# Performance work log

Hardware: AMD Instinct MI355X
Metric: run time of the kernel (lower is better)

Reference implementation:

```python
import jax, jax.numpy as jnp
import numpy as np

# ---- config (mirrors RPN __init__ + TEST proposal config) ----
B, DIN, CH, H, W = 4, 1024, 512, 50, 76
STRIDE = 16
PRE_NMS, POST_NMS = 6000, 300
NMS_THRESH, MIN_SIZE = 0.7, 16.0


def _generate_anchor_bases(base_size=16, ratios=np.array([0.5, 1.0, 2.0]), scales=np.array([8.0, 16.0, 32.0])):
    """Standard py-faster-rcnn generate_anchors."""
    def whctrs(a):
        w = a[2] - a[0] + 1.0
        h = a[3] - a[1] + 1.0
        return w, h, a[0] + 0.5 * (w - 1.0), a[1] + 0.5 * (h - 1.0)

    def mk(ws, hs, xc, yc):
        ws = ws[:, None]; hs = hs[:, None]
        return np.hstack([xc - 0.5 * (ws - 1), yc - 0.5 * (hs - 1),
                          xc + 0.5 * (ws - 1), yc + 0.5 * (hs - 1)])

    base = np.array([0.0, 0.0, base_size - 1.0, base_size - 1.0])
    w, h, xc, yc = whctrs(base)
    size = w * h
    ws = np.round(np.sqrt(size / ratios)); hs = np.round(ws * ratios)
    ratio_anchors = mk(ws, hs, xc, yc)
    out = []
    for i in range(ratio_anchors.shape[0]):
        w, h, xc, yc = whctrs(ratio_anchors[i])
        out.append(mk(w * scales, h * scales, xc, yc))
    return np.vstack(out).astype(np.float32)

ANCHOR_BASES = _generate_anchor_bases()  # [A,4]
A = ANCHOR_BASES.shape[0]                # 9


def setup_inputs() -> dict:
    keys = jax.random.split(jax.random.key(0), 4)
    base_feat = jax.random.normal(keys[0], (B, DIN, H, W), jnp.float32)
    im_info = jnp.tile(jnp.array([H * STRIDE, W * STRIDE, 1.0], jnp.float32), (B, 1))  # (im_h, im_w, scale)
    gt_boxes = jnp.zeros((B, 20, 5), jnp.float32)  # unused by forward
    num_boxes = jnp.zeros((B,), jnp.int32)         # unused by forward
    conv_w = jax.random.normal(keys[1], (CH, DIN, 3, 3), jnp.float32) * (1.0 / np.sqrt(DIN * 9))
    conv_b = jnp.zeros((CH,), jnp.float32)
    cls_w = jax.random.normal(keys[2], (2 * A, CH, 1, 1), jnp.float32) * 0.01
    cls_b = jnp.zeros((2 * A,), jnp.float32)
    bbox_w = jax.random.normal(keys[3], (4 * A, CH, 1, 1), jnp.float32) * 0.01
    bbox_b = jnp.zeros((4 * A,), jnp.float32)
    return dict(base_feat=base_feat, im_info=im_info, gt_boxes=gt_boxes, num_boxes=num_boxes,
                conv_w=conv_w, conv_b=conv_b, cls_w=cls_w, cls_b=cls_b, bbox_w=bbox_w, bbox_b=bbox_b)


def _greedy_nms(boxes, scores, n_keep, thresh):
    # boxes [N,4] (already sorted candidates), scores [N]; returns keep indices [n_keep]
    areas = (boxes[:, 2] - boxes[:, 0] + 1.0) * (boxes[:, 3] - boxes[:, 1] + 1.0)

    def body(i, st):
        sm, keep = st
        j = jnp.argmax(sm)
        keep = keep.at[i].set(j.astype(jnp.int32))
        b = boxes[j]
        xx1 = jnp.maximum(b[0], boxes[:, 0]); yy1 = jnp.maximum(b[1], boxes[:, 1])
        xx2 = jnp.minimum(b[2], boxes[:, 2]); yy2 = jnp.minimum(b[3], boxes[:, 3])
        inter = jnp.maximum(0.0, xx2 - xx1 + 1.0) * jnp.maximum(0.0, yy2 - yy1 + 1.0)
        iou = inter / (areas[j] + areas - inter)
        sm = jnp.where(iou > thresh, -jnp.inf, sm)  # suppresses j itself too (IoU=1)
        return sm, keep

    _, keep = jax.lax.fori_loop(0, n_keep, body, (scores, jnp.zeros((n_keep,), jnp.int32)))
    return keep


def reference(base_feat, im_info, gt_boxes, num_boxes, conv_w, conv_b, cls_w, cls_b, bbox_w, bbox_b):
    # 3x3 conv + relu
    x = jax.lax.conv_general_dilated(base_feat, conv_w, (1, 1), 'SAME',
                                     dimension_numbers=('NCHW', 'OIHW', 'NCHW'))
    x = jax.nn.relu(x + conv_b[None, :, None, None])
    # 1x1 heads
    cls = jnp.einsum('bchw,oc->bohw', x, cls_w[:, :, 0, 0]) + cls_b[None, :, None, None]   # [B,2A,H,W]
    bbox = jnp.einsum('bchw,oc->bohw', x, bbox_w[:, :, 0, 0]) + bbox_b[None, :, None, None]  # [B,4A,H,W]
    Bn, _, Hn, Wn = cls.shape
    # reshape(x,2)+softmax(dim=1)+reshape back == softmax over the (bg,fg) pair per anchor
    prob = jax.nn.softmax(cls.reshape(Bn, 2, A, Hn, Wn), axis=1)
    fg = prob[:, 1].transpose(0, 2, 3, 1).reshape(Bn, -1)            # [B, H*W*A], (h,w,a) order
    deltas = bbox.transpose(0, 2, 3, 1).reshape(Bn, -1, 4)           # [B, H*W*A, 4]

    # anchors in (h,w,a) order to match score/delta layout
    sy, sx = jnp.meshgrid(jnp.arange(Hn, dtype=jnp.float32) * STRIDE,
                          jnp.arange(Wn, dtype=jnp.float32) * STRIDE, indexing='ij')
    shifts = jnp.stack([sx, sy, sx, sy], -1)                         # [H,W,4]
    anchors = (shifts[:, :, None, :] + jnp.asarray(ANCHOR_BASES)[None, None]).reshape(-1, 4)
    aw = anchors[:, 2] - anchors[:, 0] + 1.0
    ah = anchors[:, 3] - anchors[:, 1] + 1.0
    axc = anchors[:, 0] + 0.5 * aw
    ayc = anchors[:, 1] + 0.5 * ah

    def per_image(scores, dl, info):
        # bbox_transform_inv
        cx = axc + dl[:, 0] * aw
        cy = ayc + dl[:, 1] * ah
        pw = jnp.exp(dl[:, 2]) * aw
        ph = jnp.exp(dl[:, 3]) * ah
        x1 = cx - 0.5 * pw; y1 = cy - 0.5 * ph
        x2 = cx + 0.5 * pw; y2 = cy + 0.5 * ph
        # clip to image
        x1 = jnp.clip(x1, 0.0, info[1] - 1.0); x2 = jnp.clip(x2, 0.0, info[1] - 1.0)
        y1 = jnp.clip(y1, 0.0, info[0] - 1.0); y2 = jnp.clip(y2, 0.0, info[0] - 1.0)
        # min_size filter (mask instead of removal to keep shapes static)
        ws = x2 - x1 + 1.0; hs = y2 - y1 + 1.0
        ms = MIN_SIZE * info[2]
        sc = jnp.where((ws >= ms) & (hs >= ms), scores, -jnp.inf)
        # pre-NMS top-k
        sc_top, idx = jax.lax.top_k(sc, PRE_NMS)
        boxes_k = jnp.stack([x1, y1, x2, y2], -1)[idx]               # [PRE_NMS,4]
        keep = _greedy_nms(boxes_k, sc_top, POST_NMS, NMS_THRESH)
        return sc_top[keep], boxes_k[keep]

    rpn_scores, rpn_bbox = jax.vmap(per_image)(fg, deltas, im_info)
    return rpn_scores[..., None], rpn_bbox  # [B,POST_NMS,1], [B,POST_NMS,4]
```

## Files before the change

kernel.cpp:

```cpp
#include <hip/hip_runtime.h>
#include <cstdint>
#include <math.h>

#define NBATCH 4
#define HH 50
#define WW 76
#define HWPIX 3800
#define HPAD 3840
#define NPROP 34200
#define NSORT 65536
#define PRE 6000
#define POST 300
#define NWORD 94
#define NROWP 6016

typedef double double4v __attribute__((ext_vector_type(4)));

__device__ __constant__ double d_AB[9][4] = {
  {-84.0,-40.0,99.0,55.0},
  {-176.0,-88.0,191.0,103.0},
  {-360.0,-184.0,375.0,199.0},
  {-56.0,-56.0,71.0,71.0},
  {-120.0,-120.0,135.0,135.0},
  {-248.0,-248.0,263.0,263.0},
  {-36.0,-80.0,51.0,95.0},
  {-80.0,-168.0,95.0,183.0},
  {-168.0,-344.0,183.0,359.0}
};

__global__ void transpose_w(const float* __restrict__ src, float* __restrict__ dst){
  __shared__ float t[32][33];
  const int kb = blockIdx.x*32, ob = blockIdx.y*32;
  const int lx = threadIdx.x, ly = threadIdx.y;
  #pragma unroll
  for (int m = 0; m < 32; m += 8){
    t[ly+m][lx] = src[(size_t)(ob+ly+m)*9216 + kb + lx];
  }
  __syncthreads();
  #pragma unroll
  for (int m = 0; m < 32; m += 8){
    dst[(size_t)(kb+ly+m)*512 + ob + lx] = t[lx][ly+m];
  }
}

__global__ void prep_head_w(const float* __restrict__ cls_w, const float* __restrict__ bbox_w,
                            float* __restrict__ wh){
  int g = blockIdx.x*256 + threadIdx.x;
  if (g >= 512*64) return;
  int c = g >> 6, o = g & 63;
  float v = 0.0f;
  if (o < 18) v = cls_w[o*512 + c];
  else if (o < 54) v = bbox_w[(o-18)*512 + c];
  wh[g] = v;
}

__global__ __launch_bounds__(256, 3) void conv3x3_mfma(
    const float* __restrict__ in, const float* __restrict__ wt,
    const float* __restrict__ bias, float* __restrict__ xout)
{
  __shared__ __align__(16) double wA[2][2304];
  __shared__ __align__(16) double iA[2][504];
  const int tid  = threadIdx.x;
  const int wave = tid >> 6, lane = tid & 63;
  const int kq = lane >> 4;
  const int ln = lane & 15;
  const int sp = blockIdx.x;
  const int rt = sp / 5, ct = sp - rt*5;
  const int y0 = rt*5, x0 = ct*16;
  const int ocb = blockIdx.y;
  const int b = blockIdx.z;
  const float* inb = in + (size_t)b*1024*HWPIX;

  int orow[4], ocol[4];
  {
    double pa  = (double)(1 << ln);
    double msk = (kq == 0) ? 1.0 : 0.0;
    double4v z = {0.0, 0.0, 0.0, 0.0};
    double4v d1 = __builtin_amdgcn_mfma_f64_16x16x4f64(pa,  msk, z, 0, 0, 0);
    double4v d2 = __builtin_amdgcn_mfma_f64_16x16x4f64(msk, pa,  z, 0, 0, 0);
    #pragma unroll
    for (int e = 0; e < 4; ++e){
      orow[e] = (int)(((__double_as_longlong(d1[e]) >> 52) & 0x7FF) - 1023);
      ocol[e] = (int)(((__double_as_longlong(d2[e]) >> 52) & 0x7FF) - 1023);
    }
  }

  double4v acc[5];
  #pragma unroll
  for (int r = 0; r < 5; ++r){ acc[r][0]=0.0; acc[r][1]=0.0; acc[r][2]=0.0; acc[r][3]=0.0; }

  float wr[9], ir[2];

  auto load_chunk = [&](int icb){
    #pragma unroll
    for (int s = 0; s < 9; ++s){
      int m = tid + s*256;
      int row = m >> 6, oc = m & 63;
      wr[s] = wt[(size_t)(icb*9 + row)*512 + ocb*64 + oc];
    }
    #pragma unroll
    for (int s = 0; s < 2; ++s){
      int m = tid + s*256;
      if (m < 504){
        int ic = m/126; int rem = m - ic*126;
        int ry = rem/18; int rx = rem - ry*18;
        int y = y0 - 1 + ry; int x = x0 - 1 + rx;
        ir[s] = ((unsigned)y < (unsigned)HH && (unsigned)x < (unsigned)WW)
                  ? inb[(size_t)(icb+ic)*HWPIX + y*WW + x] : 0.0f;
      }
    }
  };
  auto store_chunk = [&](int buf){
    #pragma unroll
    for (int s = 0; s < 9; ++s) wA[buf][tid + s*256] = (double)wr[s];
    #pragma unroll
    for (int s = 0; s < 2; ++s){
      int m = tid + s*256;
      if (m < 504) iA[buf][m] = (double)ir[s];
    }
  };

  load_chunk(0);
  store_chunk(0);
  load_chunk(4);
  __syncthreads();

  #pragma unroll 1
  for (int c = 0; c < 256; ++c){
    const int cur = c & 1;
    if (c + 1 < 256){
      store_chunk(1 - cur);
      if (c + 2 < 256) load_chunk((c + 2)*4);
    }
    #pragma unroll
    for (int tap = 0; tap < 9; ++tap){
      const int ky = tap/3, kx = tap - ky*3;
      double a = wA[cur][(kq*9 + tap)*64 + wave*16 + ln];
      #pragma unroll
      for (int rr = 0; rr < 5; ++rr){
        double bb = iA[cur][kq*126 + (rr+ky)*18 + ln + kx];
        acc[rr] = __builtin_amdgcn_mfma_f64_16x16x4f64(a, bb, acc[rr], 0, 0, 0);
      }
    }
    __syncthreads();
  }

  #pragma unroll
  for (int rr = 0; rr < 5; ++rr){
    const int y = y0 + rr;
    #pragma unroll
    for (int e = 0; e < 4; ++e){
      const int oc = ocb*64 + wave*16 + orow[e];
      const int xx = x0 + ocol[e];
      if (xx < WW){
        double val = fmax(acc[rr][e] + (double)bias[oc], 0.0);
        xout[((size_t)b*512 + oc)*HWPIX + y*WW + xx] = (float)val;
      }
    }
  }
}

__global__ __launch_bounds__(256) void head_mm(const float* __restrict__ x,
    const float* __restrict__ wh, double* __restrict__ hout)
{
  __shared__ float xs[32*128];
  __shared__ float wls[32*64];
  const int tid = threadIdx.x;
  const int b = blockIdx.y;
  const int p0 = blockIdx.x*128;
  const int oct = tid >> 5;
  const int pq = tid & 31;
  double acc[8][4];
  #pragma unroll
  for (int k=0;k<8;++k){
    #pragma unroll
    for (int j=0;j<4;++j) acc[k][j]=0.0;
  }
  const float* xb = x + (size_t)b*512*HWPIX;
  #pragma unroll 1
  for (int cb = 0; cb < 512; cb += 32){
    for (int m = tid; m < 4096; m += 256){
      int cc = m >> 7; int px = m & 127;
      int p = p0 + px;
      xs[m] = (p < HWPIX) ? xb[(size_t)(cb+cc)*HWPIX + p] : 0.0f;
    }
    for (int m = tid; m < 2048; m += 256)
      wls[m] = wh[(size_t)(cb + (m >> 6))*64 + (m & 63)];
    __syncthreads();
    #pragma unroll 1
    for (int cc = 0; cc < 32; ++cc){
      const float4 xv = *(const float4*)&xs[cc*128 + pq*4];
      double xd0 = (double)xv.x, xd1 = (double)xv.y, xd2 = (double)xv.z, xd3 = (double)xv.w;
      const float* wp = &wls[cc*64 + oct*8];
      #pragma unroll
      for (int k = 0; k < 8; ++k){
        double w = (double)wp[k];
        acc[k][0] = fma(w, xd0, acc[k][0]);
        acc[k][1] = fma(w, xd1, acc[k][1]);
        acc[k][2] = fma(w, xd2, acc[k][2]);
        acc[k][3] = fma(w, xd3, acc[k][3]);
      }
    }
    __syncthreads();
  }
  #pragma unroll
  for (int k = 0; k < 8; ++k){
    #pragma unroll
    for (int j = 0; j < 4; ++j)
      hout[((size_t)b*64 + oct*8 + k)*HPAD + p0 + pq*4 + j] = acc[k][j];
  }
}

__global__ void decode_boxes(const double* __restrict__ hout, const float* __restrict__ im_info,
    const float* __restrict__ cls_b, const float* __restrict__ bbox_b,
    double* __restrict__ sc, double* __restrict__ bxs, ulonglong2* __restrict__ keys)
{
  int g = blockIdx.x*256 + threadIdx.x;
  int b = g >> 16;
  int n = g & 65535;
  if (b >= NBATCH) return;
  ulonglong2 kv;
  if (n < NPROP){
    int p = n / 9; int a = n - p*9;
    int yr = p / WW; int xc = p - yr*WW;
    const double* hb = hout + (size_t)b*64*HPAD;
    double l0 = hb[(size_t)a*HPAD + p] + (double)cls_b[a];
    double l1 = hb[(size_t)(9+a)*HPAD + p] + (double)cls_b[9+a];
    double score = 1.0/(1.0 + exp(l0 - l1));
    double d0 = hb[(size_t)(18+4*a+0)*HPAD+p] + (double)bbox_b[4*a+0];
    double d1 = hb[(size_t)(18+4*a+1)*HPAD+p] + (double)bbox_b[4*a+1];
    double d2 = hb[(size_t)(18+4*a+2)*HPAD+p] + (double)bbox_b[4*a+2];
    double d3 = hb[(size_t)(18+4*a+3)*HPAD+p] + (double)bbox_b[4*a+3];
    double sx = 16.0*xc, sy = 16.0*yr;
    double ax1 = d_AB[a][0]+sx, ay1 = d_AB[a][1]+sy;
    double ax2 = d_AB[a][2]+sx, ay2 = d_AB[a][3]+sy;
    double aw = ax2-ax1+1.0, ah = ay2-ay1+1.0;
    double axc = ax1+0.5*aw, ayc = ay1+0.5*ah;
    double cx = axc + d0*aw, cy = ayc + d1*ah;
    double pw = exp(d2)*aw, ph = exp(d3)*ah;
    double i0 = (double)im_info[b*3+0];
    double i1 = (double)im_info[b*3+1];
    double i2 = (double)im_info[b*3+2];
    double x1 = cx - 0.5*pw, y1 = cy - 0.5*ph;
    double x2 = cx + 0.5*pw, y2 = cy + 0.5*ph;
    x1 = fmin(fmax(x1, 0.0), i1-1.0);
    x2 = fmin(fmax(x2, 0.0), i1-1.0);
    y1 = fmin(fmax(y1, 0.0), i0-1.0);
    y2 = fmin(fmax(y2, 0.0), i0-1.0);
    double wsz = x2-x1+1.0, hsz = y2-y1+1.0;
    double ms = 16.0*i2;
    double s = (wsz >= ms && hsz >= ms) ? score : -INFINITY;
    sc[(size_t)b*NPROP + n] = s;
    double* bp = bxs + ((size_t)b*NPROP + n)*4;
    bp[0]=x1; bp[1]=y1; bp[2]=x2; bp[3]=y2;
    unsigned long long u = (unsigned long long)__double_as_longlong(s);
    unsigned long long mm = (u >> 63) ? ~u : (u | 0x8000000000000000ULL);
    kv.x = ~mm; kv.y = (unsigned long long)n;
  } else {
    kv.x = ~0ULL; kv.y = (unsigned long long)n;
  }
  keys[(size_t)b*NSORT + n] = kv;
}

__device__ __forceinline__ bool kgt(const ulonglong2& a, const ulonglong2& b){
  return (a.x > b.x) || (a.x == b.x && a.y > b.y);
}
__global__ __launch_bounds__(1024) void sort_local(ulonglong2* __restrict__ keys){
  const int c = blockIdx.x & 31;
  const int b = blockIdx.x >> 5;
  ulonglong2* base = keys + (size_t)b*NSORT + c*2048;
  __shared__ ulonglong2 L[2048];
  const int tid = threadIdx.x;
  L[tid] = base[tid]; L[tid+1024] = base[tid+1024];
  __syncthreads();
  for (int k = 2; k <= 2048; k <<= 1){
    for (int j = k>>1; j > 0; j >>= 1){
      int i = ((tid & ~(j-1)) << 1) | (tid & (j-1));
      int l = i | j;
      bool asc = (((c*2048 + i) & k) == 0);
      ulonglong2 A = L[i], Bv = L[l];
      if (kgt(A,Bv) == asc){ L[i] = Bv; L[l] = A; }
      __syncthreads();
    }
  }
  base[tid] = L[tid]; base[tid+1024] = L[tid+1024];
}
__global__ void sort_gstep(ulonglong2* __restrict__ keys, int k, int j){
  int gid = blockIdx.x*256 + threadIdx.x;
  int b = gid >> 15;
  int q = gid & 32767;
  ulonglong2* base = keys + (size_t)b*NSORT;
  int i = ((q & ~(j-1)) << 1) | (q & (j-1));
  int l = i | j;
  bool asc = ((i & k) == 0);
  ulonglong2 A = base[i], Bv = base[l];
  if (kgt(A,Bv) == asc){ base[i] = Bv; base[l] = A; }
}
__global__ __launch_bounds__(1024) void sort_lmerge(ulonglong2* __restrict__ keys, int k){
  const int c = blockIdx.x & 31;
  const int b = blockIdx.x >> 5;
  ulonglong2* base = keys + (size_t)b*NSORT + c*2048;
  __shared__ ulonglong2 L[2048];
  const int tid = threadIdx.x;
  L[tid] = base[tid]; L[tid+1024] = base[tid+1024];
  __syncthreads();
  for (int j = 1024; j > 0; j >>= 1){
    int i = ((tid & ~(j-1)) << 1) | (tid & (j-1));
    int l = i | j;
    bool asc = (((c*2048 + i) & k) == 0);
    ulonglong2 A = L[i], Bv = L[l];
    if (kgt(A,Bv) == asc){ L[i] = Bv; L[l] = A; }
    __syncthreads();
  }
  base[tid] = L[tid]; base[tid+1024] = L[tid+1024];
}

__global__ void gather_top(const ulonglong2* __restrict__ keys, const double* __restrict__ sc,
    const double* __restrict__ bxs, double* __restrict__ tsc, double* __restrict__ tbx)
{
  int r = blockIdx.x*256 + threadIdx.x;
  int b = blockIdx.y;
  if (r >= PRE) return;
  int idx = (int)keys[(size_t)b*NSORT + r].y;
  tsc[(size_t)b*PRE + r] = sc[(size_t)b*NPROP + idx];
  const double* sp = bxs + ((size_t)b*NPROP + idx)*4;
  double* dp = tbx + ((size_t)b*PRE + r)*4;
  dp[0]=sp[0]; dp[1]=sp[1]; dp[2]=sp[2]; dp[3]=sp[3];
}

__global__ __launch_bounds__(64) void nms_iou_rows(const double* __restrict__ tbx,
    unsigned long long* __restrict__ rows)
{
  const int w = blockIdx.x, icx = blockIdx.y, b = blockIdx.z;
  const int i = icx*64 + threadIdx.x;
  const int ii = i < PRE ? i : PRE-1;
  const double* bp = tbx + ((size_t)b*PRE + ii)*4;
  const double x1 = bp[0], y1 = bp[1], x2 = bp[2], y2 = bp[3];
  const double ai = (x2-x1+1.0)*(y2-y1+1.0);
  const int j0 = w*64;
  const int jn = (PRE - j0) < 64 ? (PRE - j0) : 64;
  unsigned long long bits = 0;
  for (int jj = 0; jj < jn; ++jj){
    const double* qp = tbx + ((size_t)b*PRE + j0 + jj)*4;
    double qx1 = qp[0], qy1 = qp[1], qx2 = qp[2], qy2 = qp[3];
    double xx1 = fmax(x1, qx1), yy1 = fmax(y1, qy1);
    double xx2 = fmin(x2, qx2), yy2 = fmin(y2, qy2);
    double inter = fmax(0.0, xx2-xx1+1.0) * fmax(0.0, yy2-yy1+1.0);
    double aj = (qx2-qx1+1.0)*(qy2-qy1+1.0);
    double iou = inter / (ai + aj - inter);
    if (iou > 0.7) bits |= (1ULL << jj);
  }
  rows[((size_t)b*NROWP + i)*NWORD + w] = bits;
}

__global__ __launch_bounds__(128) void nms_walk(const unsigned long long* __restrict__ rows,
    const double* __restrict__ tsc, const double* __restrict__ tbx, float* __restrict__ out)
{
  const int b = blockIdx.x;
  const int tid = threadIdx.x;
  __shared__ unsigned long long W[NWORD];
  __shared__ int s_p;
  if (tid < NWORD) W[tid] = 0ULL;
  __syncthreads();
  int f = 0;
  bool exhausted = false;
  for (int it = 0; it < POST; ++it){
    if (tid == 0){
      int p = 0;
      if (!exhausted){
        int w = f >> 6;
        bool found = false;
        while (w < NWORD){
          unsigned long long valid = (w == NWORD-1) ? ((1ULL << (PRE - 64*(NWORD-1))) - 1ULL) : ~0ULL;
          unsigned long long fr = ~W[w] & valid;
          if (w == (f >> 6)) fr &= (~0ULL << (f & 63));
          if (fr){ p = w*64 + __ffsll((unsigned long long)fr) - 1; found = true; break; }
          ++w;
        }
        if (!found){ exhausted = true; p = 0; }
        else f = p + 1;
      }
      s_p = p;
    }
    __syncthreads();
    const int p = s_p;
    if (tid == 4) out[b*POST + it] = (float)tsc[(size_t)b*PRE + p];
    if (tid < 4)  out[NBATCH*POST + (size_t)(b*POST + it)*4 + tid]
                    = (float)tbx[((size_t)b*PRE + p)*4 + tid];
    if (tid < NWORD) W[tid] |= rows[((size_t)b*NROWP + p)*NWORD + tid];
    __syncthreads();
  }
}

extern "C" void kernel_launch(void* const* d_in, const int* in_sizes, int n_in,
                              void* d_out, int out_size, void* d_ws, size_t ws_size,
                              hipStream_t stream) {
  (void)in_sizes; (void)n_in; (void)out_size; (void)ws_size;
  const float* base_feat = (const float*)d_in[0];
  const float* im_info   = (const float*)d_in[1];
  const float* conv_w = (const float*)d_in[4];
  const float* conv_b = (const float*)d_in[5];
  const float* cls_w  = (const float*)d_in[6];
  const float* cls_b  = (const float*)d_in[7];
  const float* bbox_w = (const float*)d_in[8];
  const float* bbox_b = (const float*)d_in[9];
  float* out = (float*)d_out;
  char* ws = (char*)d_ws;

  float*      w_t  = (float*)     (ws + 0);
  float*      xbuf = (float*)     (ws + 18874368);
  float*      wh   = (float*)     (ws + 50003968);
  double*     hout = (double*)    (ws + 50135040);
  double*     scb  = (double*)    (ws + 57999360);
  double*     bxb  = (double*)    (ws + 59093760);
  ulonglong2* keys = (ulonglong2*)(ws + 63471360);
  double*     tops = (double*)    (ws + 67665664);
  double*     topb = (double*)    (ws + 67857664);
  unsigned long long* rows = (unsigned long long*)(ws + 0);

  transpose_w <<<dim3(288,16), dim3(32,8), 0, stream>>>(conv_w, w_t);
  prep_head_w <<<128, 256, 0, stream>>>(cls_w, bbox_w, wh);
  conv3x3_mfma<<<dim3(50,8,4), 256, 0, stream>>>(base_feat, w_t, conv_b, xbuf);
  head_mm     <<<dim3(30,4), 256, 0, stream>>>(xbuf, wh, hout);
  decode_boxes<<<1024, 256, 0, stream>>>(hout, im_info, cls_b, bbox_b, scb, bxb, keys);

  sort_local  <<<128, 1024, 0, stream>>>(keys);
  for (int k = 4096; k <= 65536; k <<= 1){
    for (int j = k>>1; j >= 2048; j >>= 1)
      sort_gstep<<<512, 256, 0, stream>>>(keys, k, j);
    sort_lmerge<<<128, 1024, 0, stream>>>(keys, k);
  }

  gather_top  <<<dim3(24,4), 256, 0, stream>>>(keys, scb, bxb, tops, topb);
  nms_iou_rows<<<dim3(NWORD,NWORD,NBATCH), 64, 0, stream>>>(topb, rows);
  nms_walk    <<<NBATCH, 128, 0, stream>>>(rows, tops, topb, out);
}
```

Baseline: 3.342 ms.

## Share conv weight tiles across batch images and fuse bitonic global sort steps

The 3x3 conv kernel now handles all four images per block with a 2-row spatial tile, so each weight chunk loaded into LDS feeds 4x more MFMAs. This cuts redundant weight traffic, at the cost of more accumulators and lower occupancy (launch bounds go from 3 to 2 blocks). Separately, consecutive global bitonic sort stages are fused into 4-element and 8-element register networks. This reduces the number of global passes and kernel launches for the sort.

After: 3.122 ms. -6.6%, faster.

```diff
diff --git a/kernel.cpp b/kernel.cpp
--- a/kernel.cpp
+++ b/kernel.cpp
@@ -54,22 +54,20 @@
   wh[g] = v;
 }
 
-__global__ __launch_bounds__(256, 3) void conv3x3_mfma(
+__global__ __launch_bounds__(256, 2) void conv3x3_mfma(
     const float* __restrict__ in, const float* __restrict__ wt,
     const float* __restrict__ bias, float* __restrict__ xout)
 {
   __shared__ __align__(16) double wA[2][2304];
-  __shared__ __align__(16) double iA[2][504];
+  __shared__ __align__(16) double iA[2][1152];
   const int tid  = threadIdx.x;
   const int wave = tid >> 6, lane = tid & 63;
   const int kq = lane >> 4;
   const int ln = lane & 15;
   const int sp = blockIdx.x;
   const int rt = sp / 5, ct = sp - rt*5;
-  const int y0 = rt*5, x0 = ct*16;
+  const int y0 = rt*2, x0 = ct*16;
   const int ocb = blockIdx.y;
-  const int b = blockIdx.z;
-  const float* inb = in + (size_t)b*1024*HWPIX;
 
   int orow[4], ocol[4];
   {
@@ -85,11 +83,14 @@
     }
   }
 
-  double4v acc[5];
-  #pragma unroll
-  for (int r = 0; r < 5; ++r){ acc[r][0]=0.0; acc[r][1]=0.0; acc[r][2]=0.0; acc[r][3]=0.0; }
-
-  float wr[9], ir[2];
+  double4v acc[4][2];
+  #pragma unroll
+  for (int g = 0; g < 4; ++g){
+    #pragma unroll
+    for (int r = 0; r < 2; ++r){ acc[g][r][0]=0.0; acc[g][r][1]=0.0; acc[g][r][2]=0.0; acc[g][r][3]=0.0; }
+  }
+
+  float wr[9], ir[5];
 
   auto load_chunk = [&](int icb){
     #pragma unroll
@@ -99,14 +100,15 @@
       wr[s] = wt[(size_t)(icb*9 + row)*512 + ocb*64 + oc];
     }
     #pragma unroll
-    for (int s = 0; s < 2; ++s){
+    for (int s = 0; s < 5; ++s){
       int m = tid + s*256;
-      if (m < 504){
-        int ic = m/126; int rem = m - ic*126;
-        int ry = rem/18; int rx = rem - ry*18;
+      if (m < 1152){
+        int img = m/288; int rem = m - img*288;
+        int ic = rem/72; int r2 = rem - ic*72;
+        int ry = r2/18; int rx = r2 - ry*18;
         int y = y0 - 1 + ry; int x = x0 - 1 + rx;
         ir[s] = ((unsigned)y < (unsigned)HH && (unsigned)x < (unsigned)WW)
-                  ? inb[(size_t)(icb+ic)*HWPIX + y*WW + x] : 0.0f;
+                  ? in[((size_t)img*1024 + icb + ic)*HWPIX + y*WW + x] : 0.0f;
       }
     }
   };
@@ -114,9 +116,9 @@
     #pragma unroll
     for (int s = 0; s < 9; ++s) wA[buf][tid + s*256] = (double)wr[s];
     #pragma unroll
-    for (int s = 0; s < 2; ++s){
+    for (int s = 0; s < 5; ++s){
       int m = tid + s*256;
-      if (m < 504) iA[buf][m] = (double)ir[s];
+      if (m < 1152) iA[buf][m] = (double)ir[s];
     }
   };
 
@@ -137,24 +139,30 @@
       const int ky = tap/3, kx = tap - ky*3;
       double a = wA[cur][(kq*9 + tap)*64 + wave*16 + ln];
       #pragma unroll
-      for (int rr = 0; rr < 5; ++rr){
-        double bb = iA[cur][kq*126 + (rr+ky)*18 + ln + kx];
-        acc[rr] = __builtin_amdgcn_mfma_f64_16x16x4f64(a, bb, acc[rr], 0, 0, 0);
+      for (int img = 0; img < 4; ++img){
+        #pragma unroll
+        for (int rr = 0; rr < 2; ++rr){
+          double bb = iA[cur][img*288 + kq*72 + (rr+ky)*18 + ln + kx];
+          acc[img][rr] = __builtin_amdgcn_mfma_f64_16x16x4f64(a, bb, acc[img][rr], 0, 0, 0);
+        }
       }
     }
     __syncthreads();
   }
 
   #pragma unroll
-  for (int rr = 0; rr < 5; ++rr){
-    const int y = y0 + rr;
-    #pragma unroll
-    for (int e = 0; e < 4; ++e){
-      const int oc = ocb*64 + wave*16 + orow[e];
-      const int xx = x0 + ocol[e];
-      if (xx < WW){
-        double val = fmax(acc[rr][e] + (double)bias[oc], 0.0);
-        xout[((size_t)b*512 + oc)*HWPIX + y*WW + xx] = (float)val;
+  for (int img = 0; img < 4; ++img){
+    #pragma unroll
+    for (int rr = 0; rr < 2; ++rr){
+      const int y = y0 + rr;
+      #pragma unroll
+      for (int e = 0; e < 4; ++e){
+        const int oc = ocb*64 + wave*16 + orow[e];
+        const int xx = x0 + ocol[e];
+        if (xx < WW){
+          double val = fmax(acc[img][rr][e] + (double)bias[oc], 0.0);
+          xout[((size_t)img*512 + oc)*HWPIX + y*WW + xx] = (float)val;
+        }
       }
     }
   }
@@ -296,6 +304,51 @@
   ulonglong2 A = base[i], Bv = base[l];
   if (kgt(A,Bv) == asc){ base[i] = Bv; base[l] = A; }
 }
+__global__ void sort_gstep2(ulonglong2* __restrict__ keys, int k, int h, int s){
+  int gid = blockIdx.x*256 + threadIdx.x;
+  int b = gid >> 14;
+  int q = gid & 16383;
+  ulonglong2* base = keys + (size_t)b*NSORT;
+  int i0 = ((q >> s) << (s+2)) | (q & (h-1));
+  bool asc = ((i0 & k) == 0);
+  ulonglong2 e0 = base[i0], e1 = base[i0+h], e2 = base[i0+2*h], e3 = base[i0+3*h];
+  ulonglong2 t;
+  if (kgt(e0,e2) == asc){ t=e0; e0=e2; e2=t; }
+  if (kgt(e1,e3) == asc){ t=e1; e1=e3; e3=t; }
+  if (kgt(e0,e1) == asc){ t=e0; e0=e1; e1=t; }
+  if (kgt(e2,e3) == asc){ t=e2; e2=e3; e3=t; }
+  base[i0]=e0; base[i0+h]=e1; base[i0+2*h]=e2; base[i0+3*h]=e3;
+}
+__global__ void sort_gstep3(ulonglong2* __restrict__ keys, int k, int h, int s){
+  int gid = blockIdx.x*256 + threadIdx.x;
+  int b = gid >> 13;
+  int q = gid & 8191;
+  ulonglong2* base = keys + (size_t)b*NSORT;
+  int i0 = ((q >> s) << (s+3)) | (q & (h-1));
+  bool asc = ((i0 & k) == 0);
+  ulonglong2 e[8];
+  #pragma unroll
+  for (int t = 0; t < 8; ++t) e[t] = base[i0 + t*h];
+  ulonglong2 t;
+  #pragma unroll
+  for (int a = 0; a < 4; ++a){
+    if (kgt(e[a],e[a+4]) == asc){ t=e[a]; e[a]=e[a+4]; e[a+4]=t; }
+  }
+  #pragma unroll
+  for (int g = 0; g < 2; ++g){
+    #pragma unroll
+    for (int a = 0; a < 2; ++a){
+      int u = g*4 + a;
+      if (kgt(e[u],e[u+2]) == asc){ t=e[u]; e[u]=e[u+2]; e[u+2]=t; }
+    }
+  }
+  #pragma unroll
+  for (int u = 0; u < 8; u += 2){
+    if (kgt(e[u],e[u+1]) == asc){ t=e[u]; e[u]=e[u+1]; e[u+1]=t; }
+  }
+  #pragma unroll
+  for (int t2 = 0; t2 < 8; ++t2) base[i0 + t2*h] = e[t2];
+}
 __global__ __launch_bounds__(1024) void sort_lmerge(ulonglong2* __restrict__ keys, int k){
   const int c = blockIdx.x & 31;
   const int b = blockIdx.x >> 5;
@@ -420,16 +473,23 @@
 
   transpose_w <<<dim3(288,16), dim3(32,8), 0, stream>>>(conv_w, w_t);
   prep_head_w <<<128, 256, 0, stream>>>(cls_w, bbox_w, wh);
-  conv3x3_mfma<<<dim3(50,8,4), 256, 0, stream>>>(base_feat, w_t, conv_b, xbuf);
+  conv3x3_mfma<<<dim3(125,8), 256, 0, stream>>>(base_feat, w_t, conv_b, xbuf);
   head_mm     <<<dim3(30,4), 256, 0, stream>>>(xbuf, wh, hout);
   decode_boxes<<<1024, 256, 0, stream>>>(hout, im_info, cls_b, bbox_b, scb, bxb, keys);
 
   sort_local  <<<128, 1024, 0, stream>>>(keys);
-  for (int k = 4096; k <= 65536; k <<= 1){
-    for (int j = k>>1; j >= 2048; j >>= 1)
-      sort_gstep<<<512, 256, 0, stream>>>(keys, k, j);
-    sort_lmerge<<<128, 1024, 0, stream>>>(keys, k);
-  }
+  sort_gstep  <<<512, 256, 0, stream>>>(keys, 4096, 2048);
+  sort_lmerge <<<128, 1024, 0, stream>>>(keys, 4096);
+  sort_gstep2 <<<256, 256, 0, stream>>>(keys, 8192, 2048, 11);
+  sort_lmerge <<<128, 1024, 0, stream>>>(keys, 8192);
+  sort_gstep3 <<<128, 256, 0, stream>>>(keys, 16384, 2048, 11);
+  sort_lmerge <<<128, 1024, 0, stream>>>(keys, 16384);
+  sort_gstep3 <<<128, 256, 0, stream>>>(keys, 32768, 4096, 12);
+  sort_gstep  <<<512, 256, 0, stream>>>(keys, 32768, 2048);
+  sort_lmerge <<<128, 1024, 0, stream>>>(keys, 32768);
+  sort_gstep3 <<<128, 256, 0, stream>>>(keys, 65536, 8192, 13);
+  sort_gstep2 <<<256, 256, 0, stream>>>(keys, 65536, 2048, 11);
+  sort_lmerge <<<128, 1024, 0, stream>>>(keys, 65536);
 
   gather_top  <<<dim3(24,4), 256, 0, stream>>>(keys, scb, bxb, tops, topb);
   nms_iou_rows<<<dim3(NWORD,NWORD,NBATCH), 64, 0, stream>>>(topb, rows);
```
